# Kernel tuning notes

Measured on AMD Instinct MI355X. Metric: run time of the kernel, lower is better.

Reference implementation:

```python
import jax, jax.numpy as jnp
import numpy as np

D_MODEL, D_FF, N_EXPERTS, TOP_K = 1024, 4096, 8, 2
BATCH, SEQ = 2, 2048


def setup_inputs() -> dict:
    key = jax.random.key(0)
    ks = jax.random.split(key, 4)
    s_in = 1.0 / np.sqrt(D_MODEL)
    s_ff = 1.0 / np.sqrt(D_FF)
    return {
        "x": jax.random.normal(ks[0], (BATCH, SEQ, D_MODEL), dtype=jnp.float32),
        "Wr": jax.random.normal(ks[1], (D_MODEL, N_EXPERTS), dtype=jnp.float32) * s_in,
        "br": jnp.zeros((N_EXPERTS,), dtype=jnp.float32),
        "W1": jax.random.normal(ks[2], (N_EXPERTS, D_MODEL, D_FF), dtype=jnp.float32) * s_in,
        "b1": jnp.zeros((N_EXPERTS, D_FF), dtype=jnp.float32),
        "W2": jax.random.normal(ks[3], (N_EXPERTS, D_FF, D_MODEL), dtype=jnp.float32) * s_ff,
        "b2": jnp.zeros((N_EXPERTS, D_MODEL), dtype=jnp.float32),
    }


def reference(x, Wr, br, W1, b1, W2, b2):
    B, S, D = x.shape
    E = Wr.shape[1]
    xf = x.reshape(-1, D)  # [T, D]

    # Router: softmax over experts, top-2, renormalize selected weights
    probs = jax.nn.softmax(xf @ Wr + br, axis=-1)            # [T, E]
    top_w, top_i = jax.lax.top_k(probs, TOP_K)               # [T, k]
    top_w = top_w / jnp.sum(top_w, axis=-1, keepdims=True)

    onehot = jax.nn.one_hot(top_i, E, dtype=xf.dtype)        # [T, k, E]
    util = onehot.mean(axis=(0, 1))                          # [E]
    combine = jnp.einsum('tk,tke->te', top_w, onehot)        # [T, E]

    # Grouped expert MLP over all tokens, then weighted combine
    h = jax.nn.gelu(jnp.einsum('td,edf->etf', xf, W1) + b1[:, None, :],
                    approximate=False)                       # [E, T, F]
    y = jnp.einsum('etf,efd->etd', h, W2) + b2[:, None, :]   # [E, T, D]
    out = jnp.einsum('te,etd->td', combine, y).reshape(B, S, D)

    # Aux load-balance loss: squared coefficient of variation (unbiased std)
    cv = jnp.std(util, ddof=1) / (jnp.mean(util) + 1e-6)
    return out, cv ** 2
```

## Files before the change

kernel.cpp:

```cpp
#include <hip/hip_runtime.h>
#include <hip/hip_bf16.h>

#define T_TOK 4096
#define DM 1024
#define DF 4096
#define NE 8

typedef __attribute__((ext_vector_type(4))) float f32x4;
typedef __attribute__((ext_vector_type(8))) short bf16x8;

__device__ inline unsigned short f2bf(float f) {
  union { float f; unsigned u; } a; a.f = f;
  unsigned r = a.u + 0x7fffu + ((a.u >> 16) & 1u);
  return (unsigned short)(r >> 16);
}
__device__ inline unsigned pk(float lo, float hi) {
  return (unsigned)f2bf(lo) | ((unsigned)f2bf(hi) << 16);
}
__device__ inline float bf2f(unsigned short u) {
  union { unsigned u; float f; } a; a.u = ((unsigned)u) << 16; return a.f;
}

__device__ inline void gload16(const void* g, void* l) {
  __builtin_amdgcn_global_load_lds(
      (const __attribute__((address_space(1))) unsigned int*)g,
      (__attribute__((address_space(3))) unsigned int*)l, 16, 0, 0);
}

__global__ __launch_bounds__(256) void k_router(const float* __restrict__ x,
    const float* __restrict__ Wr, const float* __restrict__ br,
    int* __restrict__ topi, float* __restrict__ topw, int* __restrict__ counts) {
  int t = blockIdx.x;
  int tid = threadIdx.x;
  const float* xr = x + (size_t)t * DM;
  float acc[NE];
#pragma unroll
  for (int e = 0; e < NE; e++) acc[e] = 0.f;
  for (int d = tid; d < DM; d += 256) {
    float xv = xr[d];
    const float* w = Wr + (size_t)d * NE;
#pragma unroll
    for (int e = 0; e < NE; e++) acc[e] += xv * w[e];
  }
  __shared__ float red[NE][256];
#pragma unroll
  for (int e = 0; e < NE; e++) red[e][tid] = acc[e];
  __syncthreads();
  for (int s = 128; s > 0; s >>= 1) {
    if (tid < s) {
#pragma unroll
      for (int e = 0; e < NE; e++) red[e][tid] += red[e][tid + s];
    }
    __syncthreads();
  }
  if (tid == 0) {
    float l[NE];
#pragma unroll
    for (int e = 0; e < NE; e++) l[e] = red[e][0] + br[e];
    int i0 = 0;
#pragma unroll
    for (int e = 1; e < NE; e++) if (l[e] > l[i0]) i0 = e;
    int i1 = (i0 == 0) ? 1 : 0;
#pragma unroll
    for (int e = 0; e < NE; e++) if (e != i0 && l[e] > l[i1]) i1 = e;
    float w1e = expf(l[i1] - l[i0]);
    float w0 = 1.f / (1.f + w1e);
    topi[2 * t] = i0; topi[2 * t + 1] = i1;
    topw[2 * t] = w0; topw[2 * t + 1] = w1e * w0;
    atomicAdd(&counts[i0], 1);
    atomicAdd(&counts[i1], 1);
  }
}

__global__ void k_scan(const int* __restrict__ counts, int* __restrict__ offsets,
                       float* __restrict__ cv2out) {
  if (threadIdx.x == 0) {
    int off = 0;
    float util[NE];
    for (int e = 0; e < NE; e++) { offsets[e] = off; off += counts[e]; }
    offsets[NE] = off;
    float mean = 0.f;
    for (int e = 0; e < NE; e++) { util[e] = (float)counts[e] / (float)(2 * T_TOK); mean += util[e]; }
    mean *= (1.f / NE);
    float var = 0.f;
    for (int e = 0; e < NE; e++) { float d = util[e] - mean; var += d * d; }
    var *= (1.f / (NE - 1));
    float den = mean + 1e-6f;
    *cv2out = var / (den * den);
  }
}

__global__ __launch_bounds__(256) void k_scatter(const int* __restrict__ topi,
    const int* __restrict__ offsets, int* __restrict__ cursor,
    int* __restrict__ perm, int* __restrict__ tslot) {
  int t = blockIdx.x * 256 + threadIdx.x;
  if (t >= T_TOK) return;
#pragma unroll
  for (int k = 0; k < 2; k++) {
    int e = topi[2 * t + k];
    int p = atomicAdd(&cursor[e], 1);
    int s = offsets[e] + p;
    perm[s] = t;
    tslot[2 * t + k] = s;
  }
}

__global__ __launch_bounds__(256) void k_cvtx(const float* __restrict__ x,
    unsigned short* __restrict__ xc) {
  size_t i = ((size_t)blockIdx.x * 256 + threadIdx.x) * 8;
  f32x4 a = *(const f32x4*)(x + i);
  f32x4 b = *(const f32x4*)(x + i + 4);
  uint4 v;
  v.x = pk(a[0], a[1]); v.y = pk(a[2], a[3]);
  v.z = pk(b[0], b[1]); v.w = pk(b[2], b[3]);
  *(uint4*)(xc + i) = v;
}

__global__ __launch_bounds__(256) void k_cvtT(const float* __restrict__ src,
    unsigned short* __restrict__ dst, int K, int N) {
  int e = blockIdx.z;
  int n0 = blockIdx.x * 64, k0 = blockIdx.y * 64;
  int tid = threadIdx.x;
  __shared__ float tile[64][65];
  const float* s = src + (size_t)e * K * N + (size_t)k0 * N + n0;
  int r0 = tid >> 4, c4 = (tid & 15) * 4;
#pragma unroll
  for (int i = 0; i < 4; i++) {
    int r = r0 + i * 16;
    float4 v = *(const float4*)(s + (size_t)r * N + c4);
    tile[r][c4] = v.x; tile[r][c4 + 1] = v.y; tile[r][c4 + 2] = v.z; tile[r][c4 + 3] = v.w;
  }
  __syncthreads();
  int n = tid >> 2, kc = (tid & 3) * 16;
  unsigned o[8];
#pragma unroll
  for (int j = 0; j < 8; j++)
    o[j] = pk(tile[kc + 2 * j][n], tile[kc + 2 * j + 1][n]);
  unsigned short* dp = dst + (size_t)e * N * K + (size_t)(n0 + n) * K + k0 + kc;
  *(uint4*)dp = make_uint4(o[0], o[1], o[2], o[3]);
  *(uint4*)(dp + 8) = make_uint4(o[4], o[5], o[6], o[7]);
}

__global__ __launch_bounds__(256) void k_gemm1(const unsigned short* __restrict__ xc,
    const unsigned short* __restrict__ W1t, const float* __restrict__ b1,
    const int* __restrict__ offsets, const int* __restrict__ perm,
    unsigned short* __restrict__ hb) {
  int e = blockIdx.z;
  int roff = offsets[e];
  int nrows = offsets[e + 1] - roff;
  int row_base = blockIdx.y * 128;
  if (row_base >= nrows) return;
  int n0 = blockIdx.x * 128;
  int tid = threadIdx.x, lane = tid & 63, wid = tid >> 6;
  int wm = (wid >> 1) * 64, wn = (wid & 1) * 64;

  __shared__ __align__(16) unsigned short smA[128 * 64];
  __shared__ __align__(16) unsigned short smB[128 * 64];
  __shared__ int tok_s[128];
  if (tid < 128) {
    int r = row_base + tid;
    tok_s[tid] = (r < nrows) ? perm[roff + r] : 0;
  }
  __syncthreads();

  f32x4 acc[4][4];
#pragma unroll
  for (int m = 0; m < 4; m++)
#pragma unroll
    for (int n = 0; n < 4; n++) acc[m][n] = (f32x4)(0.f);

  const unsigned short* Bbase = W1t + (size_t)e * DF * DM + (size_t)n0 * DM;

  const unsigned short* aP[4];
  const unsigned short* bP[4];
  unsigned short* lA[4];
  unsigned short* lB[4];
#pragma unroll
  for (int i = 0; i < 4; i++) {
    int c = tid + i * 256;
    int row = c >> 3;
    int o = ((c & 7) ^ (row & 7)) * 8;
    aP[i] = xc + (size_t)tok_s[row] * DM + o;
    bP[i] = Bbase + (size_t)row * DM + o;
    lA[i] = smA + c * 8;
    lB[i] = smB + c * 8;
  }

  for (int kk = 0; kk < DM / 64; kk++) {
    int k0 = kk * 64;
#pragma unroll
    for (int i = 0; i < 4; i++) {
      gload16(aP[i] + k0, lA[i]);
      gload16(bP[i] + k0, lB[i]);
    }
    __syncthreads();
#pragma unroll
    for (int ks = 0; ks < 2; ks++) {
      bf16x8 af[4], bfr[4];
#pragma unroll
      for (int m = 0; m < 4; m++) {
        int row = wm + m * 16 + (lane & 15);
        int col = ks * 64 + (lane >> 4) * 16;
        af[m] = *(const bf16x8*)((const char*)smA + row * 128 + (col ^ ((row & 7) << 4)));
      }
#pragma unroll
      for (int n = 0; n < 4; n++) {
        int row = wn + n * 16 + (lane & 15);
        int col = ks * 64 + (lane >> 4) * 16;
        bfr[n] = *(const bf16x8*)((const char*)smB + row * 128 + (col ^ ((row & 7) << 4)));
      }
#pragma unroll
      for (int m = 0; m < 4; m++)
#pragma unroll
        for (int n = 0; n < 4; n++)
          acc[m][n] = __builtin_amdgcn_mfma_f32_16x16x32_bf16(af[m], bfr[n], acc[m][n], 0, 0, 0);
    }
    __syncthreads();
  }

#pragma unroll
  for (int n = 0; n < 4; n++) {
    int col = n0 + wn + n * 16 + (lane & 15);
    float b1v = b1[e * DF + col];
#pragma unroll
    for (int m = 0; m < 4; m++) {
      int rbase = wm + m * 16 + ((lane >> 4) << 2);
#pragma unroll
      for (int r = 0; r < 4; r++) {
        int grow = row_base + rbase + r;
        if (grow < nrows) {
          float v = acc[m][n][r] + b1v;
          float g = 0.5f * v * (1.f + erff(v * 0.70710678118f));
          hb[(size_t)(roff + grow) * DF + col] = f2bf(g);
        }
      }
    }
  }
}

__global__ __launch_bounds__(256) void k_gemm2(const unsigned short* __restrict__ hb,
    const unsigned short* __restrict__ W2t, const int* __restrict__ offsets,
    unsigned short* __restrict__ y) {
  int e = blockIdx.z;
  int roff = offsets[e];
  int nrows = offsets[e + 1] - roff;
  int row_base = blockIdx.y * 128;
  if (row_base >= nrows) return;
  int n0 = blockIdx.x * 128;
  int tid = threadIdx.x, lane = tid & 63, wid = tid >> 6;
  int wm = (wid >> 1) * 64, wn = (wid & 1) * 64;

  __shared__ __align__(16) unsigned short smA[128 * 64];
  __shared__ __align__(16) unsigned short smB[128 * 64];

  f32x4 acc[4][4];
#pragma unroll
  for (int m = 0; m < 4; m++)
#pragma unroll
    for (int n = 0; n < 4; n++) acc[m][n] = (f32x4)(0.f);

  const unsigned short* Abase = hb + (size_t)(roff + row_base) * DF;
  const unsigned short* Bbase = W2t + (size_t)e * DM * DF + (size_t)n0 * DF;

  const unsigned short* aP[4];
  const unsigned short* bP[4];
  unsigned short* lA[4];
  unsigned short* lB[4];
#pragma unroll
  for (int i = 0; i < 4; i++) {
    int c = tid + i * 256;
    int row = c >> 3;
    int o = ((c & 7) ^ (row & 7)) * 8;
    aP[i] = Abase + (size_t)row * DF + o;
    bP[i] = Bbase + (size_t)row * DF + o;
    lA[i] = smA + c * 8;
    lB[i] = smB + c * 8;
  }

  for (int kk = 0; kk < DF / 64; kk++) {
    int k0 = kk * 64;
#pragma unroll
    for (int i = 0; i < 4; i++) {
      gload16(aP[i] + k0, lA[i]);
      gload16(bP[i] + k0, lB[i]);
    }
    __syncthreads();
#pragma unroll
    for (int ks = 0; ks < 2; ks++) {
      bf16x8 af[4], bfr[4];
#pragma unroll
      for (int m = 0; m < 4; m++) {
        int row = wm + m * 16 + (lane & 15);
        int col = ks * 64 + (lane >> 4) * 16;
        af[m] = *(const bf16x8*)((const char*)smA + row * 128 + (col ^ ((row & 7) << 4)));
      }
#pragma unroll
      for (int n = 0; n < 4; n++) {
        int row = wn + n * 16 + (lane & 15);
        int col = ks * 64 + (lane >> 4) * 16;
        bfr[n] = *(const bf16x8*)((const char*)smB + row * 128 + (col ^ ((row & 7) << 4)));
      }
#pragma unroll
      for (int m = 0; m < 4; m++)
#pragma unroll
        for (int n = 0; n < 4; n++)
          acc[m][n] = __builtin_amdgcn_mfma_f32_16x16x32_bf16(af[m], bfr[n], acc[m][n], 0, 0, 0);
    }
    __syncthreads();
  }

#pragma unroll
  for (int m = 0; m < 4; m++) {
    int rbase = wm + m * 16 + ((lane >> 4) << 2);
#pragma unroll
    for (int r = 0; r < 4; r++) {
      int grow = row_base + rbase + r;
      if (grow < nrows) {
#pragma unroll
        for (int n = 0; n < 4; n++) {
          int col = n0 + wn + n * 16 + (lane & 15);
          y[(size_t)(roff + grow) * DM + col] = f2bf(acc[m][n][r]);
        }
      }
    }
  }
}

__global__ __launch_bounds__(256) void k_combine(const int* __restrict__ topi,
    const float* __restrict__ topw, const int* __restrict__ tslot,
    const unsigned short* __restrict__ y, const float* __restrict__ b2,
    float* __restrict__ out) {
  int t = blockIdx.x, tid = threadIdx.x;
  int s0 = tslot[2 * t], s1 = tslot[2 * t + 1];
  int e0 = topi[2 * t], e1 = topi[2 * t + 1];
  float w0 = topw[2 * t], w1 = topw[2 * t + 1];
  int d = tid * 4;
  uint2 ya = *(const uint2*)(y + (size_t)s0 * DM + d);
  uint2 yb = *(const uint2*)(y + (size_t)s1 * DM + d);
  f32x4 bb0 = *(const f32x4*)(b2 + (size_t)e0 * DM + d);
  f32x4 bb1 = *(const f32x4*)(b2 + (size_t)e1 * DM + d);
  f32x4 r;
  r[0] = w0 * (bf2f((unsigned short)(ya.x & 0xffff)) + bb0[0]) + w1 * (bf2f((unsigned short)(yb.x & 0xffff)) + bb1[0]);
  r[1] = w0 * (bf2f((unsigned short)(ya.x >> 16)) + bb0[1]) + w1 * (bf2f((unsigned short)(yb.x >> 16)) + bb1[1]);
  r[2] = w0 * (bf2f((unsigned short)(ya.y & 0xffff)) + bb0[2]) + w1 * (bf2f((unsigned short)(yb.y & 0xffff)) + bb1[2]);
  r[3] = w0 * (bf2f((unsigned short)(ya.y >> 16)) + bb0[3]) + w1 * (bf2f((unsigned short)(yb.y >> 16)) + bb1[3]);
  *(f32x4*)(out + (size_t)t * DM + d) = r;
}

extern "C" void kernel_launch(void* const* d_in, const int* in_sizes, int n_in,
                              void* d_out, int out_size, void* d_ws, size_t ws_size,
                              hipStream_t stream) {
  const float* x  = (const float*)d_in[0];
  const float* Wr = (const float*)d_in[1];
  const float* br = (const float*)d_in[2];
  const float* W1 = (const float*)d_in[3];
  const float* b1 = (const float*)d_in[4];
  const float* W2 = (const float*)d_in[5];
  const float* b2 = (const float*)d_in[6];
  float* out = (float*)d_out;

  char* ws = (char*)d_ws;
  int*   counts  = (int*)(ws + 0);
  int*   cursor  = (int*)(ws + 64);
  int*   offsets = (int*)(ws + 128);
  int*   topi    = (int*)(ws + 256);
  float* topw    = (float*)(ws + 33024);
  int*   perm    = (int*)(ws + 65792);
  int*   tslot   = (int*)(ws + 98560);
  unsigned short* xc  = (unsigned short*)(ws + 164096);
  unsigned short* hb  = (unsigned short*)(ws + 8552704);
  unsigned short* y   = (unsigned short*)(ws + 75661568);
  unsigned short* W1t = (unsigned short*)(ws + 92438784);
  unsigned short* W2t = (unsigned short*)(ws + 159547648);

  hipMemsetAsync(ws, 0, 256, stream);

  k_cvtx<<<T_TOK * DM / (256 * 8), 256, 0, stream>>>(x, xc);
  k_cvtT<<<dim3(DF / 64, DM / 64, NE), 256, 0, stream>>>(W1, W1t, DM, DF);
  k_cvtT<<<dim3(DM / 64, DF / 64, NE), 256, 0, stream>>>(W2, W2t, DF, DM);
  k_router<<<T_TOK, 256, 0, stream>>>(x, Wr, br, topi, topw, counts);
  k_scan<<<1, 64, 0, stream>>>(counts, offsets, out + (size_t)T_TOK * DM);
  k_scatter<<<16, 256, 0, stream>>>(topi, offsets, cursor, perm, tslot);
  k_gemm1<<<dim3(32, 32, 8), 256, 0, stream>>>(xc, W1t, b1, offsets, perm, hb);
  k_gemm2<<<dim3(8, 32, 8), 256, 0, stream>>>(hb, W2t, offsets, y);
  k_combine<<<T_TOK, 256, 0, stream>>>(topi, topw, tslot, y, b2, out);
}
```

Measured before the change: 784.2 us.

## Double-buffer LDS tiles in both expert GEMMs to overlap loads with MFMA

Both grouped GEMM kernels now use two LDS buffers per operand. The next K-tile is issued via global_load_lds before computing on the current one, using an explicit vmcnt wait and raw s_barrier/sched_barrier instead of two __syncthreads per iteration. Swizzled LDS read offsets are precomputed once outside the loop. This hides global-load latency behind the MFMA work, but doubles LDS use to 64KB per block, which can lower occupancy.

```diff
diff --git a/kernel.cpp b/kernel.cpp
--- a/kernel.cpp
+++ b/kernel.cpp
@@ -141,6 +141,7 @@
   *(uint4*)(dp + 8) = make_uint4(o[4], o[5], o[6], o[7]);
 }
 
+
 __global__ __launch_bounds__(256) void k_gemm1(const unsigned short* __restrict__ xc,
     const unsigned short* __restrict__ W1t, const float* __restrict__ b1,
     const int* __restrict__ offsets, const int* __restrict__ perm,
@@ -154,8 +155,8 @@
   int tid = threadIdx.x, lane = tid & 63, wid = tid >> 6;
   int wm = (wid >> 1) * 64, wn = (wid & 1) * 64;
 
-  __shared__ __align__(16) unsigned short smA[128 * 64];
-  __shared__ __align__(16) unsigned short smB[128 * 64];
+  __shared__ __align__(16) unsigned short smA[2][128 * 64];
+  __shared__ __align__(16) unsigned short smB[2][128 * 64];
   __shared__ int tok_s[128];
   if (tid < 128) {
     int r = row_base + tid;
@@ -173,8 +174,7 @@
 
   const unsigned short* aP[4];
   const unsigned short* bP[4];
-  unsigned short* lA[4];
-  unsigned short* lB[4];
+  int ldsOff[4];
 #pragma unroll
   for (int i = 0; i < 4; i++) {
     int c = tid + i * 256;
@@ -182,41 +182,65 @@
     int o = ((c & 7) ^ (row & 7)) * 8;
     aP[i] = xc + (size_t)tok_s[row] * DM + o;
     bP[i] = Bbase + (size_t)row * DM + o;
-    lA[i] = smA + c * 8;
-    lB[i] = smB + c * 8;
-  }
-
-  for (int kk = 0; kk < DM / 64; kk++) {
-    int k0 = kk * 64;
-#pragma unroll
-    for (int i = 0; i < 4; i++) {
-      gload16(aP[i] + k0, lA[i]);
-      gload16(bP[i] + k0, lB[i]);
+    ldsOff[i] = c * 8;
+  }
+  int rA[2][4], rB[2][4];
+#pragma unroll
+  for (int ks = 0; ks < 2; ks++) {
+#pragma unroll
+    for (int m = 0; m < 4; m++) {
+      int rowa = wm + m * 16 + (lane & 15);
+      int rowb = wn + m * 16 + (lane & 15);
+      int col = ks * 64 + (lane >> 4) * 16;
+      rA[ks][m] = rowa * 128 + (col ^ ((rowa & 7) << 4));
+      rB[ks][m] = rowb * 128 + (col ^ ((rowb & 7) << 4));
     }
-    __syncthreads();
-#pragma unroll
-    for (int ks = 0; ks < 2; ks++) {
-      bf16x8 af[4], bfr[4];
-#pragma unroll
-      for (int m = 0; m < 4; m++) {
-        int row = wm + m * 16 + (lane & 15);
-        int col = ks * 64 + (lane >> 4) * 16;
-        af[m] = *(const bf16x8*)((const char*)smA + row * 128 + (col ^ ((row & 7) << 4)));
-      }
-#pragma unroll
-      for (int n = 0; n < 4; n++) {
-        int row = wn + n * 16 + (lane & 15);
-        int col = ks * 64 + (lane >> 4) * 16;
-        bfr[n] = *(const bf16x8*)((const char*)smB + row * 128 + (col ^ ((row & 7) << 4)));
-      }
-#pragma unroll
-      for (int m = 0; m < 4; m++)
-#pragma unroll
-        for (int n = 0; n < 4; n++)
-          acc[m][n] = __builtin_amdgcn_mfma_f32_16x16x32_bf16(af[m], bfr[n], acc[m][n], 0, 0, 0);
-    }
-    __syncthreads();
-  }
+  }
+
+#define STAGE1(kk, p)                                        \
+  {                                                          \
+    int k0_ = (kk) * 64;                                     \
+    _Pragma("unroll")                                        \
+    for (int i = 0; i < 4; i++) {                            \
+      gload16(aP[i] + k0_, &smA[p][ldsOff[i]]);              \
+      gload16(bP[i] + k0_, &smB[p][ldsOff[i]]);              \
+    }                                                        \
+  }
+#define COMPUTE1(p)                                                            \
+  {                                                                            \
+    const char* A_ = (const char*)smA[p];                                      \
+    const char* B_ = (const char*)smB[p];                                      \
+    _Pragma("unroll")                                                          \
+    for (int ks = 0; ks < 2; ks++) {                                           \
+      bf16x8 af[4], bfr[4];                                                    \
+      _Pragma("unroll")                                                        \
+      for (int m = 0; m < 4; m++) af[m] = *(const bf16x8*)(A_ + rA[ks][m]);    \
+      _Pragma("unroll")                                                        \
+      for (int n = 0; n < 4; n++) bfr[n] = *(const bf16x8*)(B_ + rB[ks][n]);   \
+      _Pragma("unroll")                                                        \
+      for (int m = 0; m < 4; m++)                                              \
+        _Pragma("unroll")                                                      \
+        for (int n = 0; n < 4; n++)                                            \
+          acc[m][n] = __builtin_amdgcn_mfma_f32_16x16x32_bf16(af[m], bfr[n],   \
+                                                              acc[m][n], 0, 0, 0); \
+    }                                                                          \
+  }
+
+  STAGE1(0, 0);
+  for (int t = 0; t < DM / 64 - 1; ++t) {
+    STAGE1(t + 1, (t + 1) & 1);
+    asm volatile("s_waitcnt vmcnt(8)" ::: "memory");
+    __builtin_amdgcn_s_barrier();
+    __builtin_amdgcn_sched_barrier(0);
+    COMPUTE1(t & 1);
+    asm volatile("s_waitcnt lgkmcnt(0)" ::: "memory");
+    __builtin_amdgcn_sched_barrier(0);
+    __builtin_amdgcn_s_barrier();
+  }
+  asm volatile("s_waitcnt vmcnt(0)" ::: "memory");
+  __builtin_amdgcn_s_barrier();
+  __builtin_amdgcn_sched_barrier(0);
+  COMPUTE1((DM / 64 - 1) & 1);
 
 #pragma unroll
   for (int n = 0; n < 4; n++) {
@@ -250,8 +274,8 @@
   int tid = threadIdx.x, lane = tid & 63, wid = tid >> 6;
   int wm = (wid >> 1) * 64, wn = (wid & 1) * 64;
 
-  __shared__ __align__(16) unsigned short smA[128 * 64];
-  __shared__ __align__(16) unsigned short smB[128 * 64];
+  __shared__ __align__(16) unsigned short smA[2][128 * 64];
+  __shared__ __align__(16) unsigned short smB[2][128 * 64];
 
   f32x4 acc[4][4];
 #pragma unroll
@@ -264,8 +288,7 @@
 
   const unsigned short* aP[4];
   const unsigned short* bP[4];
-  unsigned short* lA[4];
-  unsigned short* lB[4];
+  int ldsOff[4];
 #pragma unroll
   for (int i = 0; i < 4; i++) {
     int c = tid + i * 256;
@@ -273,41 +296,65 @@
     int o = ((c & 7) ^ (row & 7)) * 8;
     aP[i] = Abase + (size_t)row * DF + o;
     bP[i] = Bbase + (size_t)row * DF + o;
-    lA[i] = smA + c * 8;
-    lB[i] = smB + c * 8;
-  }
-
-  for (int kk = 0; kk < DF / 64; kk++) {
-    int k0 = kk * 64;
-#pragma unroll
-    for (int i = 0; i < 4; i++) {
-      gload16(aP[i] + k0, lA[i]);
-      gload16(bP[i] + k0, lB[i]);
+    ldsOff[i] = c * 8;
+  }
+  int rA[2][4], rB[2][4];
+#pragma unroll
+  for (int ks = 0; ks < 2; ks++) {
+#pragma unroll
+    for (int m = 0; m < 4; m++) {
+      int rowa = wm + m * 16 + (lane & 15);
+      int rowb = wn + m * 16 + (lane & 15);
+      int col = ks * 64 + (lane >> 4) * 16;
+      rA[ks][m] = rowa * 128 + (col ^ ((rowa & 7) << 4));
+      rB[ks][m] = rowb * 128 + (col ^ ((rowb & 7) << 4));
     }
-    __syncthreads();
-#pragma unroll
-    for (int ks = 0; ks < 2; ks++) {
-      bf16x8 af[4], bfr[4];
-#pragma unroll
-      for (int m = 0; m < 4; m++) {
-        int row = wm + m * 16 + (lane & 15);
-        int col = ks * 64 + (lane >> 4) * 16;
-        af[m] = *(const bf16x8*)((const char*)smA + row * 128 + (col ^ ((row & 7) << 4)));
-      }
-#pragma unroll
-      for (int n = 0; n < 4; n++) {
-        int row = wn + n * 16 + (lane & 15);
-        int col = ks * 64 + (lane >> 4) * 16;
-        bfr[n] = *(const bf16x8*)((const char*)smB + row * 128 + (col ^ ((row & 7) << 4)));
-      }
-#pragma unroll
-      for (int m = 0; m < 4; m++)
-#pragma unroll
-        for (int n = 0; n < 4; n++)
-          acc[m][n] = __builtin_amdgcn_mfma_f32_16x16x32_bf16(af[m], bfr[n], acc[m][n], 0, 0, 0);
-    }
-    __syncthreads();
-  }
+  }
+
+#define STAGE2(kk, p)                                        \
+  {                                                          \
+    int k0_ = (kk) * 64;                                     \
+    _Pragma("unroll")                                        \
+    for (int i = 0; i < 4; i++) {                            \
+      gload16(aP[i] + k0_, &smA[p][ldsOff[i]]);              \
+      gload16(bP[i] + k0_, &smB[p][ldsOff[i]]);              \
+    }                                                        \
+  }
+#define COMPUTE2(p)                                                            \
+  {                                                                            \
+    const char* A_ = (const char*)smA[p];                                      \
+    const char* B_ = (const char*)smB[p];                                      \
+    _Pragma("unroll")                                                          \
+    for (int ks = 0; ks < 2; ks++) {                                           \
+      bf16x8 af[4], bfr[4];                                                    \
+      _Pragma("unroll")                                                        \
+      for (int m = 0; m < 4; m++) af[m] = *(const bf16x8*)(A_ + rA[ks][m]);    \
+      _Pragma("unroll")                                                        \
+      for (int n = 0; n < 4; n++) bfr[n] = *(const bf16x8*)(B_ + rB[ks][n]);   \
+      _Pragma("unroll")                                                        \
+      for (int m = 0; m < 4; m++)                                              \
+        _Pragma("unroll")                                                      \
+        for (int n = 0; n < 4; n++)                                            \
+          acc[m][n] = __builtin_amdgcn_mfma_f32_16x16x32_bf16(af[m], bfr[n],   \
+                                                              acc[m][n], 0, 0, 0); \
+    }                                                                          \
+  }
+
+  STAGE2(0, 0);
+  for (int t = 0; t < DF / 64 - 1; ++t) {
+    STAGE2(t + 1, (t + 1) & 1);
+    asm volatile("s_waitcnt vmcnt(8)" ::: "memory");
+    __builtin_amdgcn_s_barrier();
+    __builtin_amdgcn_sched_barrier(0);
+    COMPUTE2(t & 1);
+    asm volatile("s_waitcnt lgkmcnt(0)" ::: "memory");
+    __builtin_amdgcn_sched_barrier(0);
+    __builtin_amdgcn_s_barrier();
+  }
+  asm volatile("s_waitcnt vmcnt(0)" ::: "memory");
+  __builtin_amdgcn_s_barrier();
+  __builtin_amdgcn_sched_barrier(0);
+  COMPUTE2((DF / 64 - 1) & 1);
 
 #pragma unroll
   for (int m = 0; m < 4; m++) {
```

Result: no change. 799.5 us (+1.9%).
